# Kernel optimization log

Hardware: AMD Instinct MI355X
Metric: run time of the kernel (lower is better)

The kernel has to match this reference:

```python
import jax, jax.numpy as jnp
import numpy as np

B, N, F, E, D, H, L = 4, 2048, 2, 16, 32, 4, 2
GRAPH_LAYERS = 3
FLOW_ITERS = 10
COST_C = 1.0        # quadratic cost: c*x^2, inv_derivative(y) = y/(2c)
BIG_NUMBER = 1e7


def setup_inputs():
    key = jax.random.key(0)
    ks = jax.random.split(key, 20)
    node_features = jax.random.normal(ks[0], (B, N, F), jnp.float32)
    node_embeddings = jax.random.normal(ks[1], (B, N, E), jnp.float32)
    demands = jax.random.normal(ks[2], (B, N, 1), jnp.float32)
    demands = demands - demands.mean(axis=1, keepdims=True)  # flow conservation
    adj = (jax.random.uniform(ks[3], (B, N, N)) < 0.01).astype(jnp.float32)
    adj = adj * (1.0 - jnp.eye(N, dtype=jnp.float32))
    eye = jnp.broadcast_to(jnp.eye(N, dtype=jnp.float32), (B, N, N))
    neighborhoods = jnp.stack([eye, adj], axis=1)  # [B,L,N,N] hop-0 and hop-1
    def g(k, shape):
        return jax.random.normal(k, shape, jnp.float32) * 0.1
    params = {
        'We1': g(ks[4], (E + F, D)), 'be1': jnp.zeros((D,), jnp.float32),
        'We2': g(ks[5], (D, D)), 'be2': jnp.zeros((D,), jnp.float32),
        'w_attn': g(ks[6], (H, D)),
        'Wo': g(ks[7], (D, D)), 'bo': jnp.zeros((D,), jnp.float32),
        'Wz': g(ks[8], (D, D)), 'Uz': g(ks[9], (D, D)), 'bz': jnp.zeros((D,), jnp.float32),
        'Wr': g(ks[10], (D, D)), 'Ur': g(ks[11], (D, D)), 'br': jnp.zeros((D,), jnp.float32),
        'Wh': g(ks[12], (D, D)), 'Uh': g(ks[13], (D, D)), 'bh': jnp.zeros((D,), jnp.float32),
        'Wd1': g(ks[14], (D, D)), 'bd1': jnp.zeros((D,), jnp.float32),
        'Wd2': g(ks[15], (D, 1)), 'bd2': jnp.zeros((1,), jnp.float32),
        'Wv1': g(ks[16], (D, D)), 'bv1': jnp.zeros((D,), jnp.float32),
        'Wv2': g(ks[17], (D, 1)), 'bv2': jnp.zeros((1,), jnp.float32),
    }
    return {'node_features': node_features, 'node_embeddings': node_embeddings,
            'demands': demands, 'adj': adj, 'neighborhoods': neighborhoods, **params}


def _forward(node_features, node_embeddings, demands, adj, neighborhoods,
             We1, be1, We2, be2, w_attn, Wo, bo,
             Wz, Uz, bz, Wr, Ur, br, Wh, Uh, bh,
             Wd1, bd1, Wd2, bd2, Wv1, bv1, Wv2, bv2):
    # --- node encoder MLP (tanh, activate_final=True) ---
    x = jnp.concatenate([node_embeddings, node_features], axis=-1)   # [B,N,E+F]
    enc = jnp.tanh(jnp.tanh(x @ We1 + be1) @ We2 + be2)               # [B,N,D]
    # row-normalized neighborhood operators (degree-normalized aggregation)
    Mnorm = neighborhoods / (jnp.sum(neighborhoods, axis=-1, keepdims=True) + 1.0)
    # --- graph_layers x (attention neighborhood + GRU state update) ---
    for _ in range(GRAPH_LAYERS):
        agg = jnp.einsum('blnm,bmd->blnd', Mnorm, enc)                # [B,L,N,D]
        scores = jnp.einsum('blnd,hd->bhnl', jnp.tanh(agg), w_attn)   # [B,H,N,L]
        alpha = jax.nn.softmax(scores, axis=-1)
        ctx = jnp.einsum('bhnl,blnd->bnd', alpha, agg) / H            # mean over heads
        nbr = jnp.tanh(ctx @ Wo + bo)                                 # [B,N,D]
        z = jax.nn.sigmoid(nbr @ Wz + enc @ Uz + bz)
        r = jax.nn.sigmoid(nbr @ Wr + enc @ Ur + br)
        h = jnp.tanh(nbr @ Wh + (r * enc) @ Uh + bh)
        enc = z * enc + (1.0 - z) * h
    # --- primal: edge weights, masked softmax, proportional flow solver ---
    pred = (enc @ Wd1 + bd1) @ Wd2 + bd2                              # [B,N,1]
    pw = pred * jnp.transpose(pred, (0, 2, 1))                        # [B,N,N]
    weights = -BIG_NUMBER * (1.0 - adj) + pw
    fwp = jax.nn.softmax(weights, axis=-1)                            # rows sum to 1
    flow0 = fwp * jax.nn.relu(-demands)

    def step(flow, _):
        inflow = jnp.sum(flow, axis=1)[..., None]                     # [B,N,1]
        return fwp * jax.nn.relu(inflow - demands), None

    flow, _ = jax.lax.scan(step, flow0, None, length=FLOW_ITERS)
    flow_cost = jnp.sum(COST_C * flow * flow, axis=(1, 2))            # [B]
    # --- dual: dual variables, dual flows via inverse cost derivative ---
    dual = (enc @ Wv1 + bv1) @ Wv2 + bv2                              # [B,N,1]
    dd = dual - jnp.transpose(dual, (0, 2, 1))                        # [B,N,N]
    df = adj * jax.nn.relu(dd / (2.0 * COST_C))
    dual_cost = jnp.sum(COST_C * df * df - dd * df, axis=(1, 2)) \
        - jnp.sum(dual * demands, axis=(1, 2))                        # [B]
    return flow_cost - dual_cost                                      # primal-dual gap loss, [B]


def reference(node_features, node_embeddings, demands, adj, neighborhoods,
              We1, be1, We2, be2, w_attn, Wo, bo,
              Wz, Uz, bz, Wr, Ur, br, Wh, Uh, bh,
              Wd1, bd1, Wd2, bd2, Wv1, bv1, Wv2, bv2):
    return _forward(node_features, node_embeddings, demands, adj, neighborhoods,
                    We1, be1, We2, be2, w_attn, Wo, bo,
                    Wz, Uz, bz, Wr, Ur, br, Wh, Uh, bh,
                    Wd1, bd1, Wd2, bd2, Wv1, bv1, Wv2, bv2)
```

## Files before the change

### kernel.cpp

```cpp
#include <hip/hip_runtime.h>

#define NN 2048
#define NB 4
#define BN (NB * NN)
#define MAXD 96

__device__ __forceinline__ float fast_rcp(float x) { return __builtin_amdgcn_rcpf(x); }
__device__ __forceinline__ float fast_tanh(float x) {
    float a = __expf(2.0f * fabsf(x));
    float r = 1.0f - 2.0f * fast_rcp(1.0f + a);
    return copysignf(r, x);
}
__device__ __forceinline__ float fast_sigmoid(float x) {
    return fast_rcp(1.0f + __expf(-x));
}

__global__ __launch_bounds__(256) void k_front(
    const float* __restrict__ feat, const float* __restrict__ emb,
    const float* __restrict__ We1, const float* __restrict__ be1,
    const float* __restrict__ We2, const float* __restrict__ be2,
    float* __restrict__ enc_out,
    const float* __restrict__ adj, int* __restrict__ deg, int* __restrict__ cols,
    int* __restrict__ tdeg)
{
    int tid = threadIdx.x;
    if (blockIdx.x < 1024) {
        __shared__ float sW1[18 * 32], sb1[32], sW2[32 * 32], sb2[32];
        for (int i = tid; i < 18 * 32; i += 256) sW1[i] = We1[i];
        for (int i = tid; i < 32 * 32; i += 256) sW2[i] = We2[i];
        if (tid < 32) { sb1[tid] = be1[tid]; sb2[tid] = be2[tid]; }
        __syncthreads();
        int group = tid >> 5, j = tid & 31;
        int node = blockIdx.x * 8 + group;
        float x;
        if (j < 16)      x = emb[node * 16 + j];
        else if (j < 18) x = feat[node * 2 + (j - 16)];
        else             x = 0.f;
        float acc = sb1[j];
#pragma unroll
        for (int k = 0; k < 18; k++)
            acc += __shfl(x, k, 32) * sW1[k * 32 + j];
        float h = fast_tanh(acc);
        float acc2 = sb2[j];
#pragma unroll
        for (int k = 0; k < 32; k++)
            acc2 += __shfl(h, k, 32) * sW2[k * 32 + j];
        enc_out[node * 32 + j] = fast_tanh(acc2);
    } else {
        int wave = tid >> 6, lane = tid & 63;
        int row = (blockIdx.x - 1024) * 4 + wave;
        const float4* p = (const float4*)(adj + (size_t)row * NN);
        int cnt = 0;
        int base = row * MAXD;
#pragma unroll
        for (int it = 0; it < 8; it++) {
            float4 v = p[it * 64 + lane];
            float va[4] = { v.x, v.y, v.z, v.w };
#pragma unroll
            for (int c = 0; c < 4; c++) {
                unsigned long long m = __ballot(va[c] != 0.f);
                if (va[c] != 0.f) {
                    int pos = cnt + __popcll(m & ((1ull << lane) - 1ull));
                    if (pos < MAXD) cols[base + pos] = it * 256 + lane * 4 + c;
                }
                cnt += __popcll(m);
            }
        }
        if (lane == 0) {
            deg[row] = cnt < MAXD ? cnt : MAXD;
            tdeg[row] = 0;
        }
    }
}

__device__ __forceinline__ float layer_rest(
    int g, int j, float e, float a1raw, int d,
    const float4* sPack, const float2* sWhUh, const float* sWo,
    const float* sAttn, const float* sbo, const float* sbz,
    const float* sbr, const float* sbh,
    float2 (*sNE)[32], float (*sCtx)[32])
{
    float agg0 = 0.5f * e;
    float a1 = a1raw * fast_rcp((float)(d + 1));
    float t0 = fast_tanh(agg0), t1 = fast_tanh(a1);
    float td = t0 - t1;
    float s0 = sAttn[j] * td, s1 = sAttn[32 + j] * td,
          s2 = sAttn[64 + j] * td, s3 = sAttn[96 + j] * td;
#pragma unroll
    for (int off = 16; off >= 1; off >>= 1) {
        s0 += __shfl_xor(s0, off, 32);
        s1 += __shfl_xor(s1, off, 32);
        s2 += __shfl_xor(s2, off, 32);
        s3 += __shfl_xor(s3, off, 32);
    }
    float c0 = 0.25f * (fast_sigmoid(s0) + fast_sigmoid(s1) +
                        fast_sigmoid(s2) + fast_sigmoid(s3));
    float ctx = c0 * agg0 + (1.0f - c0) * a1;
    sCtx[g][j] = ctx;
    float acc = sbo[j];
#pragma unroll
    for (int k = 0; k < 32; k++)
        acc += sCtx[g][k] * sWo[k * 32 + j];
    float nbr = fast_tanh(acc);
    sNE[g][j] = make_float2(nbr, e);
    float az = sbz[j], ar = sbr[j];
#pragma unroll
    for (int k = 0; k < 32; k++) {
        float2 ne = sNE[g][k];
        float4 w  = sPack[k * 32 + j];
        az += ne.x * w.x + ne.y * w.y;
        ar += ne.x * w.z + ne.y * w.w;
    }
    float z = fast_sigmoid(az), r = fast_sigmoid(ar);
    sNE[g][j].y = r * e;
    float ah = sbh[j];
#pragma unroll
    for (int k = 0; k < 32; k++) {
        float2 ne = sNE[g][k];
        float2 wh = sWhUh[k * 32 + j];
        ah += ne.x * wh.x + ne.y * wh.y;
    }
    float hc = fast_tanh(ah);
    return z * e + (1.0f - z) * hc;
}

__device__ __forceinline__ float hop1_gather(
    int g, int j, int d, const int* __restrict__ cp,
    const float* __restrict__ encB, int (*sCols)[64])
{
    sCols[g][j]      = cp[j];
    sCols[g][j + 32] = cp[j + 32];
    float a = 0.f, b = 0.f, c = 0.f, e4 = 0.f;
    int i = 0;
    for (; i + 3 < d; i += 4) {
        int m0 = sCols[g][i],     m1 = sCols[g][i + 1];
        int m2 = sCols[g][i + 2], m3 = sCols[g][i + 3];
        a  += encB[m0 * 32 + j];
        b  += encB[m1 * 32 + j];
        c  += encB[m2 * 32 + j];
        e4 += encB[m3 * 32 + j];
    }
    for (; i < d; i++) a += encB[sCols[g][i] * 32 + j];
    return (a + b) + (c + e4);
}

__global__ __launch_bounds__(1024) void k_layer(
    const float* __restrict__ enc_in, float* __restrict__ enc_out,
    const int* __restrict__ deg, const int* __restrict__ cols,
    const float* __restrict__ w_attn,
    const float* __restrict__ Wo, const float* __restrict__ bo,
    const float* __restrict__ Wz, const float* __restrict__ Uz, const float* __restrict__ bz,
    const float* __restrict__ Wr, const float* __restrict__ Ur, const float* __restrict__ br,
    const float* __restrict__ Wh, const float* __restrict__ Uh, const float* __restrict__ bh)
{
    __shared__ float4 sPack[1024];
    __shared__ float2 sWhUh[1024];
    __shared__ float  sWo[1024];
    __shared__ float  sAttn[128], sbo[32], sbz[32], sbr[32], sbh[32];
    __shared__ int    sCols[32][64];
    __shared__ float2 sNE[32][32];
    __shared__ float  sCtx[32][32];
    int tid = threadIdx.x;
    sPack[tid] = make_float4(Wz[tid], Uz[tid], Wr[tid], Ur[tid]);
    sWhUh[tid] = make_float2(Wh[tid], Uh[tid]);
    sWo[tid] = Wo[tid];
    if (tid < 128) sAttn[tid] = w_attn[tid];
    if (tid < 32) { sbo[tid] = bo[tid]; sbz[tid] = bz[tid]; sbr[tid] = br[tid]; sbh[tid] = bh[tid]; }
    int g = tid >> 5, j = tid & 31;
    int node = blockIdx.x * 32 + g;
    int b = node >> 11;
    const float* encB = enc_in + (size_t)(b * NN) * 32;
    float e = enc_in[node * 32 + j];
    int d = deg[node];
    const int* cp = cols + node * MAXD;
    float a1 = hop1_gather(g, j, d, cp, encB, sCols);
    __syncthreads();
    float eo = layer_rest(g, j, e, a1, d, sPack, sWhUh, sWo,
                          sAttn, sbo, sbz, sbr, sbh, sNE, sCtx);
    enc_out[node * 32 + j] = eo;
}

__global__ __launch_bounds__(1024) void k_layer_last(
    const float* __restrict__ enc_in,
    const int* __restrict__ deg, const int* __restrict__ cols,
    const float* __restrict__ w_attn,
    const float* __restrict__ Wo, const float* __restrict__ bo,
    const float* __restrict__ Wz, const float* __restrict__ Uz, const float* __restrict__ bz,
    const float* __restrict__ Wr, const float* __restrict__ Ur, const float* __restrict__ br,
    const float* __restrict__ Wh, const float* __restrict__ Uh, const float* __restrict__ bh,
    const float* __restrict__ Wd1, const float* __restrict__ bd1,
    const float* __restrict__ Wd2, const float* __restrict__ bd2,
    const float* __restrict__ Wv1, const float* __restrict__ bv1,
    const float* __restrict__ Wv2, const float* __restrict__ bv2,
    float* __restrict__ pred, float* __restrict__ dual)
{
    __shared__ float4 sPack[1024];
    __shared__ float2 sWhUh[1024];
    __shared__ float2 sWdv[1024];
    __shared__ float  sWo[1024];
    __shared__ float  sAttn[128], sbo[32], sbz[32], sbr[32], sbh[32];
    __shared__ float  sbd1[32], sbv1[32], sWd2v[32], sWv2v[32];
    __shared__ int    sCols[32][64];
    __shared__ float2 sNE[32][32];
    __shared__ float  sCtx[32][32];
    int tid = threadIdx.x;
    sPack[tid] = make_float4(Wz[tid], Uz[tid], Wr[tid], Ur[tid]);
    sWhUh[tid] = make_float2(Wh[tid], Uh[tid]);
    sWdv[tid]  = make_float2(Wd1[tid], Wv1[tid]);
    sWo[tid] = Wo[tid];
    if (tid < 128) sAttn[tid] = w_attn[tid];
    if (tid < 32) {
        sbo[tid] = bo[tid]; sbz[tid] = bz[tid]; sbr[tid] = br[tid]; sbh[tid] = bh[tid];
        sbd1[tid] = bd1[tid]; sbv1[tid] = bv1[tid]; sWd2v[tid] = Wd2[tid]; sWv2v[tid] = Wv2[tid];
    }
    int g = tid >> 5, j = tid & 31;
    int node = blockIdx.x * 32 + g;
    int b = node >> 11;
    const float* encB = enc_in + (size_t)(b * NN) * 32;
    float e = enc_in[node * 32 + j];
    int d = deg[node];
    const int* cp = cols + node * MAXD;
    float a1 = hop1_gather(g, j, d, cp, encB, sCols);
    __syncthreads();
    float eo = layer_rest(g, j, e, a1, d, sPack, sWhUh, sWo,
                          sAttn, sbo, sbz, sbr, sbh, sNE, sCtx);
    sCtx[g][j] = eo;
    float ad = sbd1[j], av = sbv1[j];
#pragma unroll
    for (int k = 0; k < 32; k++) {
        float ek = sCtx[g][k];
        float2 wd = sWdv[k * 32 + j];
        ad += ek * wd.x;
        av += ek * wd.y;
    }
    float pd = ad * sWd2v[j];
    float dv = av * sWv2v[j];
#pragma unroll
    for (int off = 16; off >= 1; off >>= 1) {
        pd += __shfl_xor(pd, off, 32);
        dv += __shfl_xor(dv, off, 32);
    }
    if (j == 0) {
        pred[node] = pd + bd2[0];
        dual[node] = dv + bv2[0];
    }
}

__global__ __launch_bounds__(256) void k_edge_scatter(
    const int* __restrict__ deg, const int* __restrict__ cols,
    const float* __restrict__ pred, const float* __restrict__ dual,
    int* __restrict__ tdeg, unsigned* __restrict__ tpack,
    float* __restrict__ rowsq, float* __restrict__ rowdual)
{
    int wave = threadIdx.x >> 6, lane = threadIdx.x & 63;
    int row = blockIdx.x * 4 + wave;
    int b = row >> 11;
    int rloc = row & (NN - 1);
    const float* predB = pred + b * NN;
    const float* dualB = dual + b * NN;
    int d = deg[row];
    int base = row * MAXD;
    float pn = pred[row];
    float dn = dual[row];
    float mx = -1e30f;
    for (int i = lane; i < d; i += 64) {
        int c = cols[base + i];
        mx = fmaxf(mx, pn * predB[c]);
    }
#pragma unroll
    for (int off = 32; off >= 1; off >>= 1) mx = fmaxf(mx, __shfl_xor(mx, off));
    float den = 0.f, du = 0.f;
    for (int i = lane; i < d; i += 64) {
        int c = cols[base + i];
        den += __expf(pn * predB[c] - mx);
        float dd = dn - dualB[c];
        if (dd > 0.f) du -= 0.25f * dd * dd;
    }
#pragma unroll
    for (int off = 32; off >= 1; off >>= 1) { den += __shfl_xor(den, off); du += __shfl_xor(du, off); }
    float invden = fast_rcp(den);
    float rs = 0.f;
    for (int i = lane; i < d; i += 64) {
        int c = cols[base + i];
        float f = __expf(pn * predB[c] - mx) * invden;
        rs += f * f;
        int pos = atomicAdd(&tdeg[b * NN + c], 1);
        if (pos < MAXD) {
            unsigned wv = ((__float_as_uint(f) + 0x400u) & 0xFFFFF800u) | (unsigned)rloc;
            tpack[(size_t)(b * NN + c) * MAXD + pos] = wv;
        }
    }
#pragma unroll
    for (int off = 32; off >= 1; off >>= 1) rs += __shfl_xor(rs, off);
    if (lane == 0) { rowsq[row] = rs; rowdual[row] = du; }
}

__device__ __forceinline__ float edge_accum(
    const unsigned* __restrict__ rp, int d, const float* __restrict__ S)
{
    float p0 = 0.f, p1 = 0.f, p2 = 0.f, p3 = 0.f;
    int q = d >> 2;
#pragma unroll 2
    for (int i = 0; i < q; i++) {
        uint4 w = ((const uint4*)rp)[i];
        p0 += __uint_as_float(w.x & 0xFFFFF800u) * S[w.x & 0x7FFu];
        p1 += __uint_as_float(w.y & 0xFFFFF800u) * S[w.y & 0x7FFu];
        p2 += __uint_as_float(w.z & 0xFFFFF800u) * S[w.z & 0x7FFu];
        p3 += __uint_as_float(w.w & 0xFFFFF800u) * S[w.w & 0x7FFu];
    }
    for (int i = q << 2; i < d; i++) {
        unsigned w = rp[i];
        p0 += __uint_as_float(w & 0xFFFFF800u) * S[w & 0x7FFu];
    }
    return (p0 + p1) + (p2 + p3);
}

__global__ __launch_bounds__(1024) void k_flow_batch(
    const int* __restrict__ tdeg, const unsigned* __restrict__ tpack,
    const float* __restrict__ demands,
    const float* __restrict__ rowsq, const float* __restrict__ rowdual,
    const float* __restrict__ dual, float* __restrict__ out)
{
    __shared__ float sdem[NN], sA[NN], sBuf[NN];
    __shared__ float red[3][16];
    int tid = threadIdx.x;
    int b = blockIdx.x;
    const float* demB = demands + b * NN;
    for (int n = tid; n < NN; n += 1024) {
        float dm = demB[n];
        sdem[n] = dm;
        sA[n] = fmaxf(-dm, 0.f);
    }
    __syncthreads();
    int n0 = tid, n1 = tid + 1024;
    int d0 = tdeg[b * NN + n0];
    int d1 = tdeg[b * NN + n1];
    if (d0 > MAXD) d0 = MAXD;
    if (d1 > MAXD) d1 = MAXD;
    const unsigned* rp0 = tpack + (size_t)(b * NN + n0) * MAXD;
    const unsigned* rp1 = tpack + (size_t)(b * NN + n1) * MAXD;
    float dm0 = sdem[n0], dm1 = sdem[n1];
#pragma unroll 1
    for (int it = 0; it < 5; it++) {
        {
            float a0 = edge_accum(rp0, d0, sA);
            float a1 = edge_accum(rp1, d1, sA);
            sBuf[n0] = fmaxf(a0 - dm0, 0.f);
            sBuf[n1] = fmaxf(a1 - dm1, 0.f);
        }
        __syncthreads();
        {
            float a0 = edge_accum(rp0, d0, sBuf);
            float a1 = edge_accum(rp1, d1, sBuf);
            sA[n0] = fmaxf(a0 - dm0, 0.f);
            sA[n1] = fmaxf(a1 - dm1, 0.f);
        }
        __syncthreads();
    }
    float fc = 0.f, ds = 0.f, dq = 0.f;
    for (int n = tid; n < NN; n += 1024) {
        int row = b * NN + n;
        float sv = sA[n];
        fc += rowsq[row] * sv * sv;
        ds += rowdual[row];
        dq += dual[row] * sdem[n];
    }
#pragma unroll
    for (int off = 32; off >= 1; off >>= 1) {
        fc += __shfl_xor(fc, off);
        ds += __shfl_xor(ds, off);
        dq += __shfl_xor(dq, off);
    }
    int wv = tid >> 6;
    if ((tid & 63) == 0) { red[0][wv] = fc; red[1][wv] = ds; red[2][wv] = dq; }
    __syncthreads();
    if (tid == 0) {
        float a = 0.f, s1 = 0.f, s2 = 0.f;
        for (int w = 0; w < 16; w++) { a += red[0][w]; s1 += red[1][w]; s2 += red[2][w]; }
        out[b] = a - s1 + s2;
    }
}

extern "C" void kernel_launch(void* const* d_in, const int* in_sizes, int n_in,
                              void* d_out, int out_size, void* d_ws, size_t ws_size,
                              hipStream_t stream) {
    const float* feat = (const float*)d_in[0];
    const float* emb  = (const float*)d_in[1];
    const float* dem  = (const float*)d_in[2];
    const float* adj  = (const float*)d_in[3];
    const float* We1 = (const float*)d_in[5];
    const float* be1 = (const float*)d_in[6];
    const float* We2 = (const float*)d_in[7];
    const float* be2 = (const float*)d_in[8];
    const float* w_attn = (const float*)d_in[9];
    const float* Wo = (const float*)d_in[10];
    const float* bo = (const float*)d_in[11];
    const float* Wz = (const float*)d_in[12];
    const float* Uz = (const float*)d_in[13];
    const float* bz = (const float*)d_in[14];
    const float* Wr = (const float*)d_in[15];
    const float* Ur = (const float*)d_in[16];
    const float* br = (const float*)d_in[17];
    const float* Wh = (const float*)d_in[18];
    const float* Uh = (const float*)d_in[19];
    const float* bh = (const float*)d_in[20];
    const float* Wd1 = (const float*)d_in[21];
    const float* bd1 = (const float*)d_in[22];
    const float* Wd2 = (const float*)d_in[23];
    const float* bd2 = (const float*)d_in[24];
    const float* Wv1 = (const float*)d_in[25];
    const float* bv1 = (const float*)d_in[26];
    const float* Wv2 = (const float*)d_in[27];
    const float* bv2 = (const float*)d_in[28];
    float* out = (float*)d_out;

    float* w = (float*)d_ws;
    float* enc0 = w;            w += (size_t)BN * 32;
    float* enc1 = w;            w += (size_t)BN * 32;
    int*   degp = (int*)w;      w += BN;
    int*   colp = (int*)w;      w += (size_t)BN * MAXD;
    float* pred = w;            w += BN;
    float* dual = w;            w += BN;
    float* rowsq = w;           w += BN;
    float* rowdual = w;         w += BN;
    int*   tdeg = (int*)w;      w += BN;
    unsigned* tpk = (unsigned*)w; w += (size_t)BN * MAXD;

    k_front<<<3072, 256, 0, stream>>>(feat, emb, We1, be1, We2, be2, enc0,
                                      adj, degp, colp, tdeg);
    k_layer<<<BN / 32, 1024, 0, stream>>>(enc0, enc1, degp, colp, w_attn,
                                          Wo, bo, Wz, Uz, bz, Wr, Ur, br, Wh, Uh, bh);
    k_layer<<<BN / 32, 1024, 0, stream>>>(enc1, enc0, degp, colp, w_attn,
                                          Wo, bo, Wz, Uz, bz, Wr, Ur, br, Wh, Uh, bh);
    k_layer_last<<<BN / 32, 1024, 0, stream>>>(enc0, degp, colp, w_attn,
                                               Wo, bo, Wz, Uz, bz, Wr, Ur, br, Wh, Uh, bh,
                                               Wd1, bd1, Wd2, bd2, Wv1, bv1, Wv2, bv2,
                                               pred, dual);
    k_edge_scatter<<<BN / 4, 256, 0, stream>>>(degp, colp, pred, dual,
                                               tdeg, tpk, rowsq, rowdual);
    k_flow_batch<<<NB, 1024, 0, stream>>>(tdeg, tpk, dem,
                                          rowsq, rowdual, dual, out);
}
```

Before: 398.5 us.

## Transpose packed edge layout, fold decoder heads, add single-pass softmax scatter

Stores the transposed edge pack column-major (slot-major across nodes), so flow-iteration threads read consecutive addresses for the same slot index and the loads coalesce instead of each thread striding through its own row. Precomputes Wd1·Wd2 and Wv1·Wv2 (plus bias terms) in shared memory, since there is no nonlinearity between the two decoder layers. This turns the last-layer dense projections into a single dot product. Also adds a one-pass path in the edge-scatter kernel for rows with at most 64 neighbours, which avoids re-reading columns three times. The risks are scalar inner loops without the uint4 vectorization and reordered floating-point accumulation.

```diff
diff --git a/kernel.cpp b/kernel.cpp
--- a/kernel.cpp
+++ b/kernel.cpp
@@ -196,22 +196,36 @@
 {
     __shared__ float4 sPack[1024];
     __shared__ float2 sWhUh[1024];
-    __shared__ float2 sWdv[1024];
     __shared__ float  sWo[1024];
     __shared__ float  sAttn[128], sbo[32], sbz[32], sbr[32], sbh[32];
-    __shared__ float  sbd1[32], sbv1[32], sWd2v[32], sWv2v[32];
+    __shared__ float  swd[32], swv[32], shc[2];
     __shared__ int    sCols[32][64];
     __shared__ float2 sNE[32][32];
     __shared__ float  sCtx[32][32];
     int tid = threadIdx.x;
     sPack[tid] = make_float4(Wz[tid], Uz[tid], Wr[tid], Ur[tid]);
     sWhUh[tid] = make_float2(Wh[tid], Uh[tid]);
-    sWdv[tid]  = make_float2(Wd1[tid], Wv1[tid]);
     sWo[tid] = Wo[tid];
     if (tid < 128) sAttn[tid] = w_attn[tid];
-    if (tid < 32) {
-        sbo[tid] = bo[tid]; sbz[tid] = bz[tid]; sbr[tid] = br[tid]; sbh[tid] = bh[tid];
-        sbd1[tid] = bd1[tid]; sbv1[tid] = bv1[tid]; sWd2v[tid] = Wd2[tid]; sWv2v[tid] = Wv2[tid];
+    if (tid < 32) { sbo[tid] = bo[tid]; sbz[tid] = bz[tid]; sbr[tid] = br[tid]; sbh[tid] = bh[tid]; }
+    if (tid >= 64 && tid < 96) {
+        int k = tid - 64;
+        float a = 0.f, av = 0.f;
+#pragma unroll
+        for (int jj = 0; jj < 32; jj++) {
+            a  += Wd1[k * 32 + jj] * Wd2[jj];
+            av += Wv1[k * 32 + jj] * Wv2[jj];
+        }
+        swd[k] = a; swv[k] = av;
+    }
+    if (tid == 96) {
+        float c1 = 0.f, c2 = 0.f;
+#pragma unroll
+        for (int jj = 0; jj < 32; jj++) {
+            c1 += bd1[jj] * Wd2[jj];
+            c2 += bv1[jj] * Wv2[jj];
+        }
+        shc[0] = c1 + bd2[0]; shc[1] = c2 + bv2[0];
     }
     int g = tid >> 5, j = tid & 31;
     int node = blockIdx.x * 32 + g;
@@ -224,25 +238,16 @@
     __syncthreads();
     float eo = layer_rest(g, j, e, a1, d, sPack, sWhUh, sWo,
                           sAttn, sbo, sbz, sbr, sbh, sNE, sCtx);
-    sCtx[g][j] = eo;
-    float ad = sbd1[j], av = sbv1[j];
-#pragma unroll
-    for (int k = 0; k < 32; k++) {
-        float ek = sCtx[g][k];
-        float2 wd = sWdv[k * 32 + j];
-        ad += ek * wd.x;
-        av += ek * wd.y;
-    }
-    float pd = ad * sWd2v[j];
-    float dv = av * sWv2v[j];
+    float pd = eo * swd[j];
+    float dv = eo * swv[j];
 #pragma unroll
     for (int off = 16; off >= 1; off >>= 1) {
         pd += __shfl_xor(pd, off, 32);
         dv += __shfl_xor(dv, off, 32);
     }
     if (j == 0) {
-        pred[node] = pd + bd2[0];
-        dual[node] = dv + bv2[0];
+        pred[node] = pd + shc[0];
+        dual[node] = dv + shc[1];
     }
 }
 
@@ -262,57 +267,68 @@
     int base = row * MAXD;
     float pn = pred[row];
     float dn = dual[row];
-    float mx = -1e30f;
-    for (int i = lane; i < d; i += 64) {
-        int c = cols[base + i];
-        mx = fmaxf(mx, pn * predB[c]);
-    }
-#pragma unroll
-    for (int off = 32; off >= 1; off >>= 1) mx = fmaxf(mx, __shfl_xor(mx, off));
-    float den = 0.f, du = 0.f;
-    for (int i = lane; i < d; i += 64) {
-        int c = cols[base + i];
-        den += __expf(pn * predB[c] - mx);
-        float dd = dn - dualB[c];
-        if (dd > 0.f) du -= 0.25f * dd * dd;
-    }
-#pragma unroll
-    for (int off = 32; off >= 1; off >>= 1) { den += __shfl_xor(den, off); du += __shfl_xor(du, off); }
-    float invden = fast_rcp(den);
-    float rs = 0.f;
-    for (int i = lane; i < d; i += 64) {
-        int c = cols[base + i];
-        float f = __expf(pn * predB[c] - mx) * invden;
-        rs += f * f;
-        int pos = atomicAdd(&tdeg[b * NN + c], 1);
-        if (pos < MAXD) {
-            unsigned wv = ((__float_as_uint(f) + 0x400u) & 0xFFFFF800u) | (unsigned)rloc;
-            tpack[(size_t)(b * NN + c) * MAXD + pos] = wv;
-        }
-    }
-#pragma unroll
-    for (int off = 32; off >= 1; off >>= 1) rs += __shfl_xor(rs, off);
-    if (lane == 0) { rowsq[row] = rs; rowdual[row] = du; }
-}
-
-__device__ __forceinline__ float edge_accum(
-    const unsigned* __restrict__ rp, int d, const float* __restrict__ S)
-{
-    float p0 = 0.f, p1 = 0.f, p2 = 0.f, p3 = 0.f;
-    int q = d >> 2;
-#pragma unroll 2
-    for (int i = 0; i < q; i++) {
-        uint4 w = ((const uint4*)rp)[i];
-        p0 += __uint_as_float(w.x & 0xFFFFF800u) * S[w.x & 0x7FFu];
-        p1 += __uint_as_float(w.y & 0xFFFFF800u) * S[w.y & 0x7FFu];
-        p2 += __uint_as_float(w.z & 0xFFFFF800u) * S[w.z & 0x7FFu];
-        p3 += __uint_as_float(w.w & 0xFFFFF800u) * S[w.w & 0x7FFu];
-    }
-    for (int i = q << 2; i < d; i++) {
-        unsigned w = rp[i];
-        p0 += __uint_as_float(w & 0xFFFFF800u) * S[w & 0x7FFu];
-    }
-    return (p0 + p1) + (p2 + p3);
+    if (d <= 64) {
+        int c = 0;
+        float w = -1e30f, du = 0.f;
+        bool act = lane < d;
+        if (act) {
+            c = cols[base + lane];
+            w = pn * predB[c];
+            float dd = dn - dualB[c];
+            if (dd > 0.f) du = -0.25f * dd * dd;
+        }
+        float mx = w;
+#pragma unroll
+        for (int off = 32; off >= 1; off >>= 1) mx = fmaxf(mx, __shfl_xor(mx, off));
+        float ex = act ? __expf(w - mx) : 0.f;
+        float den = ex;
+#pragma unroll
+        for (int off = 32; off >= 1; off >>= 1) { den += __shfl_xor(den, off); du += __shfl_xor(du, off); }
+        float f = ex * fast_rcp(den);
+        float rs = f * f;
+        if (act) {
+            int pos = atomicAdd(&tdeg[b * NN + c], 1);
+            if (pos < MAXD) {
+                unsigned wv = ((__float_as_uint(f) + 0x400u) & 0xFFFFF800u) | (unsigned)rloc;
+                tpack[(size_t)(b * MAXD + pos) * NN + c] = wv;
+            }
+        } else rs = 0.f;
+#pragma unroll
+        for (int off = 32; off >= 1; off >>= 1) rs += __shfl_xor(rs, off);
+        if (lane == 0) { rowsq[row] = rs; rowdual[row] = du; }
+    } else {
+        float mx = -1e30f;
+        for (int i = lane; i < d; i += 64) {
+            int c = cols[base + i];
+            mx = fmaxf(mx, pn * predB[c]);
+        }
+#pragma unroll
+        for (int off = 32; off >= 1; off >>= 1) mx = fmaxf(mx, __shfl_xor(mx, off));
+        float den = 0.f, du = 0.f;
+        for (int i = lane; i < d; i += 64) {
+            int c = cols[base + i];
+            den += __expf(pn * predB[c] - mx);
+            float dd = dn - dualB[c];
+            if (dd > 0.f) du -= 0.25f * dd * dd;
+        }
+#pragma unroll
+        for (int off = 32; off >= 1; off >>= 1) { den += __shfl_xor(den, off); du += __shfl_xor(du, off); }
+        float invden = fast_rcp(den);
+        float rs = 0.f;
+        for (int i = lane; i < d; i += 64) {
+            int c = cols[base + i];
+            float f = __expf(pn * predB[c] - mx) * invden;
+            rs += f * f;
+            int pos = atomicAdd(&tdeg[b * NN + c], 1);
+            if (pos < MAXD) {
+                unsigned wv = ((__float_as_uint(f) + 0x400u) & 0xFFFFF800u) | (unsigned)rloc;
+                tpack[(size_t)(b * MAXD + pos) * NN + c] = wv;
+            }
+        }
+#pragma unroll
+        for (int off = 32; off >= 1; off >>= 1) rs += __shfl_xor(rs, off);
+        if (lane == 0) { rowsq[row] = rs; rowdual[row] = du; }
+    }
 }
 
 __global__ __launch_bounds__(1024) void k_flow_batch(
@@ -337,21 +353,34 @@
     int d1 = tdeg[b * NN + n1];
     if (d0 > MAXD) d0 = MAXD;
     if (d1 > MAXD) d1 = MAXD;
-    const unsigned* rp0 = tpack + (size_t)(b * NN + n0) * MAXD;
-    const unsigned* rp1 = tpack + (size_t)(b * NN + n1) * MAXD;
     float dm0 = sdem[n0], dm1 = sdem[n1];
+    const unsigned* tp = tpack + (size_t)b * MAXD * NN;
 #pragma unroll 1
     for (int it = 0; it < 5; it++) {
         {
-            float a0 = edge_accum(rp0, d0, sA);
-            float a1 = edge_accum(rp1, d1, sA);
+            float a0 = 0.f, a1 = 0.f;
+            for (int i = 0; i < d0; i++) {
+                unsigned wv = tp[i * NN + n0];
+                a0 += __uint_as_float(wv & 0xFFFFF800u) * sA[wv & 0x7FFu];
+            }
+            for (int i = 0; i < d1; i++) {
+                unsigned wv = tp[i * NN + n1];
+                a1 += __uint_as_float(wv & 0xFFFFF800u) * sA[wv & 0x7FFu];
+            }
             sBuf[n0] = fmaxf(a0 - dm0, 0.f);
             sBuf[n1] = fmaxf(a1 - dm1, 0.f);
         }
         __syncthreads();
         {
-            float a0 = edge_accum(rp0, d0, sBuf);
-            float a1 = edge_accum(rp1, d1, sBuf);
+            float a0 = 0.f, a1 = 0.f;
+            for (int i = 0; i < d0; i++) {
+                unsigned wv = tp[i * NN + n0];
+                a0 += __uint_as_float(wv & 0xFFFFF800u) * sBuf[wv & 0x7FFu];
+            }
+            for (int i = 0; i < d1; i++) {
+                unsigned wv = tp[i * NN + n1];
+                a1 += __uint_as_float(wv & 0xFFFFF800u) * sBuf[wv & 0x7FFu];
+            }
             sA[n0] = fmaxf(a0 - dm0, 0.f);
             sA[n1] = fmaxf(a1 - dm1, 0.f);
         }
```

Result: faster. 381.2 us, median of 2 (-4.3%).
